# Optimization experiments

Hardware: AMD Instinct MI355X
Metric: run time of the kernel (lower is better)

The kernel has to match this reference:

```python
import jax, jax.numpy as jnp
import numpy as np

IN_CH = 128
OUT_CH = 1
N_NODES = 20000
N_EDGES = 640000
EPS = 1e-5


def setup_inputs() -> dict:
    key = jax.random.key(0)
    ks = jax.random.split(key, 8)
    x = jax.random.normal(ks[0], (N_NODES, IN_CH), dtype=jnp.float32)
    edge_index = jax.random.randint(ks[1], (2, N_EDGES), 0, N_NODES, dtype=jnp.int64)
    s1 = 1.0 / np.sqrt(2 * IN_CH)
    s2 = 1.0 / np.sqrt(IN_CH)
    return {
        "x": x,
        "edge_index": edge_index,
        "W1": jax.random.normal(ks[2], (2 * IN_CH, IN_CH), dtype=jnp.float32) * s1,
        "b1": jnp.zeros((IN_CH,), dtype=jnp.float32),
        "bn_g": jnp.ones((IN_CH,), dtype=jnp.float32),
        "bn_b": jnp.zeros((IN_CH,), dtype=jnp.float32),
        "W2": jax.random.normal(ks[3], (IN_CH, IN_CH), dtype=jnp.float32) * s2,
        "b2": jnp.zeros((IN_CH,), dtype=jnp.float32),
        "ln_g": jnp.ones((IN_CH,), dtype=jnp.float32),
        "ln_b": jnp.zeros((IN_CH,), dtype=jnp.float32),
        "W3": jax.random.normal(ks[4], (IN_CH, OUT_CH), dtype=jnp.float32) * s2,
        "b3": jnp.zeros((OUT_CH,), dtype=jnp.float32),
    }


def gcn_conv(h, src, dst, num_nodes, bias):
    # h: [num_nodes, F] already linearly transformed. GCN norm with self loops:
    # deg[i] = 1 + in-degree(i); norm_e = deg[src]^-1/2 * deg[dst]^-1/2
    deg = jnp.zeros((num_nodes,), h.dtype).at[dst].add(1.0) + 1.0
    dinv = deg ** -0.5
    norm = dinv[src] * dinv[dst]                      # [E]
    agg = jnp.zeros_like(h).at[dst].add(h[src] * norm[:, None])
    agg = agg + h * (dinv * dinv)[:, None]            # self-loop contribution
    return agg + bias


def reference(x, edge_index, W1, b1, bn_g, bn_b, W2, b2, ln_g, ln_b, W3, b3):
    src, dst = edge_index[0], edge_index[1]
    E = src.shape[0]
    # edge features: [E, 2*IN_CH]
    ef = jnp.concatenate([x[src], x[dst]], axis=1)
    # GCNConv 1 over E "nodes" (edge-feature rows)
    h = gcn_conv(ef @ W1, src, dst, E, b1)
    # BatchNorm1d (training-mode batch stats, biased variance)
    mean = h.mean(axis=0)
    var = h.var(axis=0)
    h = (h - mean) * jax.lax.rsqrt(var + EPS) * bn_g + bn_b
    h = jax.nn.relu(h)
    # GCNConv 2
    h = gcn_conv(h @ W2, src, dst, E, b2)
    # LayerNorm over feature dim
    mu = h.mean(axis=-1, keepdims=True)
    v = h.var(axis=-1, keepdims=True)
    h = (h - mu) * jax.lax.rsqrt(v + EPS) * ln_g + ln_b
    h = jax.nn.relu(h)
    out = h @ W3 + b3                                  # [E, 1]
    return out.squeeze()
```

## Files before the change

### kernel.cpp

```cpp
#include <hip/hip_runtime.h>
#include <hip/hip_bf16.h>

#define NN 20000
#define NE 640000
#define TAILN (NE - NN)
#define F  128
#define EPSN 1e-5f

typedef __bf16 bf16;
typedef bf16  bf16x8 __attribute__((ext_vector_type(8)));
typedef bf16  bf16x4 __attribute__((ext_vector_type(4)));
typedef float f32x4  __attribute__((ext_vector_type(4)));
typedef float f32x2  __attribute__((ext_vector_type(2)));
typedef unsigned short u16;

__global__ void k_cvt_idx(const void* __restrict__ ei_raw, int* __restrict__ srcb,
                          int* __restrict__ dstb, int* __restrict__ cnt,
                          int* __restrict__ cst, int* __restrict__ cdt) {
  const int* e32 = (const int*)ei_raw;
  const long long* e64 = (const long long*)ei_raw;
  bool is64 = true;
#pragma unroll
  for (int k = 0; k < 8; ++k) is64 = is64 && (e32[2 * k + 1] == 0);
  int e = blockIdx.x * 256 + threadIdx.x;
  if (e < NE) {
    int s, d;
    if (is64) { s = (int)e64[e]; d = (int)e64[NE + e]; }
    else      { s = e32[e];      d = e32[NE + e]; }
    srcb[e] = s; dstb[e] = d;
    atomicAdd(&cnt[d], 1);
    if (e >= NN) { atomicAdd(&cst[s], 1); atomicAdd(&cdt[d], 1); }
  }
}

__global__ __launch_bounds__(256) void k1_gemm1(const float* __restrict__ x,
        const float* __restrict__ W1, bf16* __restrict__ xa, bf16* __restrict__ xb) {
  __shared__ float XT[64][129];
  int row0 = blockIdx.x * 64;
  int half = blockIdx.y >> 1;
  int cb   = (blockIdx.y & 1) * 64;
  const float* W = W1 + (size_t)half * F * F;
  bf16* out = half ? xb : xa;
  int t = threadIdx.x;
#pragma unroll
  for (int i = 0; i < 8; ++i) {
    int flat = i * 1024 + t * 4;
    int r = flat >> 7, c = flat & 127;
    int gr = row0 + r;
    f32x4 v = {0.f, 0.f, 0.f, 0.f};
    if (gr < NN) v = *(const f32x4*)(x + (size_t)gr * F + c);
    XT[r][c] = v[0]; XT[r][c + 1] = v[1]; XT[r][c + 2] = v[2]; XT[r][c + 3] = v[3];
  }
  __syncthreads();
  int tc = t & 15, tr = t >> 4;
  float acc[4][4] = {};
  for (int k = 0; k < F; ++k) {
    f32x4 wv = *(const f32x4*)(W + (size_t)k * F + cb + tc * 4);
    float x0 = XT[tr * 4 + 0][k], x1 = XT[tr * 4 + 1][k];
    float x2 = XT[tr * 4 + 2][k], x3 = XT[tr * 4 + 3][k];
#pragma unroll
    for (int j = 0; j < 4; ++j) {
      acc[0][j] += x0 * wv[j]; acc[1][j] += x1 * wv[j];
      acc[2][j] += x2 * wv[j]; acc[3][j] += x3 * wv[j];
    }
  }
#pragma unroll
  for (int i = 0; i < 4; ++i) {
    int gr = row0 + tr * 4 + i;
    if (gr < NN) {
      bf16x4 o;
#pragma unroll
      for (int j = 0; j < 4; ++j) o[j] = (bf16)acc[i][j];
      *(bf16x4*)(out + (size_t)gr * F + cb + tc * 4) = o;
    }
  }
}

__global__ __launch_bounds__(1024) void k3_scan(const int* __restrict__ cnt,
        int* __restrict__ ptr, int* __restrict__ cursor,
        float* __restrict__ dinv, float* __restrict__ invdeg) {
  __shared__ int wsum[16];
  __shared__ int carry_s;
  int t = threadIdx.x;
  int lane = t & 63, wv = t >> 6;
  if (t == 0) carry_s = 0;
  __syncthreads();
  for (int c0 = 0; c0 < NN; c0 += 1024) {
    int i = c0 + t;
    int v = (i < NN) ? cnt[i] : 0;
    int s = v;
#pragma unroll
    for (int off = 1; off < 64; off <<= 1) {
      int n = __shfl_up(s, off);
      if (lane >= off) s += n;
    }
    if (lane == 63) wsum[wv] = s;
    __syncthreads();
    int carry = carry_s;
    int wbase = 0;
#pragma unroll
    for (int k2 = 0; k2 < 16; ++k2) wbase += (k2 < wv) ? wsum[k2] : 0;
    int incl = s + wbase;
    if (i < NN) {
      int excl = carry + incl - v;
      ptr[i] = excl; cursor[i] = excl;
      float deg = (float)(v + 1);
      dinv[i] = rsqrtf(deg);
      invdeg[i] = 1.0f / deg;
    }
    __syncthreads();
    if (t == 1023) carry_s = carry + incl;
    __syncthreads();
  }
  if (t == 0) ptr[NN] = carry_s;
}

__global__ void k4_hhead(const int* __restrict__ srcb, const int* __restrict__ dstb,
                         const bf16* __restrict__ xa, const bf16* __restrict__ xb,
                         bf16* __restrict__ hh) {
  int flat = blockIdx.x * 256 + threadIdx.x;
  int j = flat >> 4, ch = flat & 15;
  if (j >= NN) return;
  int s = srcb[j], d = dstb[j];
  bf16x8 a = *(const bf16x8*)(xa + (size_t)s * F + ch * 8);
  bf16x8 b = *(const bf16x8*)(xb + (size_t)d * F + ch * 8);
  bf16x8 o;
#pragma unroll
  for (int m = 0; m < 8; ++m) o[m] = (bf16)((float)a[m] + (float)b[m]);
  *(bf16x8*)(hh + (size_t)j * F + ch * 8) = o;
}

__global__ void k5_fill(const int* __restrict__ srcb, const int* __restrict__ dstb,
                        int* __restrict__ cursor, int* __restrict__ csr_s) {
  int e = blockIdx.x * 256 + threadIdx.x;
  if (e < NE) {
    int d = dstb[e];
    int pos = atomicAdd(&cursor[d], 1);
    csr_s[pos] = srcb[e] | ((e >= NN) ? (1 << 16) : 0);
  }
}

__global__ __launch_bounds__(256) void k6_conv1cross(const int* __restrict__ ptr,
        const int* __restrict__ csr_s, const bf16* __restrict__ hh,
        const bf16* __restrict__ xa, const bf16* __restrict__ xb,
        const float* __restrict__ dinv, const float* __restrict__ invdeg,
        const float* __restrict__ b1, float* __restrict__ h1h,
        float* __restrict__ crossrow) {
  int w = threadIdx.x >> 6, lane = threadIdx.x & 63;
  int g = lane >> 4, k = lane & 15;
  int i = blockIdx.x * 4 + w;
  int c0 = k * 8;
  int beg = ptr[i], end = ptr[i + 1];
  float acc[8] = {0,0,0,0,0,0,0,0}, z[8] = {0,0,0,0,0,0,0,0};
  int q = beg + g;
  for (; q + 4 < end; q += 8) {
    int v0 = csr_s[q], v1 = csr_s[q + 4];
    int s0 = v0 & 0xFFFF, s1 = v1 & 0xFFFF;
    float f0 = (v0 >> 16) ? 1.f : 0.f, f1 = (v1 >> 16) ? 1.f : 0.f;
    float d0 = dinv[s0], d1 = dinv[s1];
    bf16x8 h0 = *(const bf16x8*)(hh + (size_t)s0 * F + c0);
    bf16x8 x0 = *(const bf16x8*)(xa + (size_t)s0 * F + c0);
    bf16x8 h1 = *(const bf16x8*)(hh + (size_t)s1 * F + c0);
    bf16x8 x1 = *(const bf16x8*)(xa + (size_t)s1 * F + c0);
#pragma unroll
    for (int j = 0; j < 8; ++j) {
      acc[j] += d0 * (float)h0[j] + d1 * (float)h1[j];
      z[j]   += f0 * (float)x0[j] + f1 * (float)x1[j];
    }
  }
  if (q < end) {
    int v0 = csr_s[q];
    int s0 = v0 & 0xFFFF;
    float f0 = (v0 >> 16) ? 1.f : 0.f;
    float d0 = dinv[s0];
    bf16x8 h0 = *(const bf16x8*)(hh + (size_t)s0 * F + c0);
    bf16x8 x0 = *(const bf16x8*)(xa + (size_t)s0 * F + c0);
#pragma unroll
    for (int j = 0; j < 8; ++j) {
      acc[j] += d0 * (float)h0[j];
      z[j]   += f0 * (float)x0[j];
    }
  }
#pragma unroll
  for (int m = 16; m < 64; m <<= 1) {
#pragma unroll
    for (int j = 0; j < 8; ++j) {
      acc[j] += __shfl_xor(acc[j], m);
      z[j]   += __shfl_xor(z[j], m);
    }
  }
  if (g == 0) {
    float di = dinv[i], iv = invdeg[i];
    bf16x8 self = *(const bf16x8*)(hh + (size_t)i * F + c0);
    f32x4 bA = *(const f32x4*)(b1 + c0), bB = *(const f32x4*)(b1 + c0 + 4);
    f32x4 o0, o1;
#pragma unroll
    for (int j = 0; j < 4; ++j) {
      o0[j] = di * acc[j]     + (float)self[j]     * iv + bA[j];
      o1[j] = di * acc[j + 4] + (float)self[j + 4] * iv + bB[j];
    }
    *(f32x4*)(h1h + (size_t)i * F + c0) = o0;
    *(f32x4*)(h1h + (size_t)i * F + c0 + 4) = o1;
  } else if (g == 1) {
    bf16x8 xbv = *(const bf16x8*)(xb + (size_t)i * F + c0);
    f32x4 o0, o1;
#pragma unroll
    for (int j = 0; j < 4; ++j) {
      o0[j] = (float)xbv[j]     * z[j];
      o1[j] = (float)xbv[j + 4] * z[j + 4];
    }
    *(f32x4*)(crossrow + (size_t)i * F + c0) = o0;
    *(f32x4*)(crossrow + (size_t)i * F + c0 + 4) = o1;
  }
}

__global__ __launch_bounds__(256) void k7sr(const float* __restrict__ h1h,
        const float* __restrict__ crossrow, const bf16* __restrict__ xa,
        const bf16* __restrict__ xb, const int* __restrict__ cst,
        const int* __restrict__ cdt, float* __restrict__ statsB) {
  int t = threadIdx.x;
  int w = t >> 6, lane = t & 63, k = lane & 15;
  int rg = t >> 4;
  int c0 = k * 8;
  int base = blockIdx.x * 200;
  float A1[8] = {0,0,0,0,0,0,0,0}, A2[8] = {0,0,0,0,0,0,0,0};
  float B1[8] = {0,0,0,0,0,0,0,0}, B2[8] = {0,0,0,0,0,0,0,0};
  float Cc[8] = {0,0,0,0,0,0,0,0};
  for (int r = rg; r < 200; r += 16) {
    int n = base + r;
    f32x4 h0 = *(const f32x4*)(h1h + (size_t)n * F + c0);
    f32x4 h1 = *(const f32x4*)(h1h + (size_t)n * F + c0 + 4);
    f32x4 cr0 = *(const f32x4*)(crossrow + (size_t)n * F + c0);
    f32x4 cr1 = *(const f32x4*)(crossrow + (size_t)n * F + c0 + 4);
    bf16x8 av = *(const bf16x8*)(xa + (size_t)n * F + c0);
    bf16x8 bv = *(const bf16x8*)(xb + (size_t)n * F + c0);
    float ca = (float)cst[n], cb = (float)cdt[n];
#pragma unroll
    for (int j = 0; j < 4; ++j) {
      A1[j] += h0[j]; A2[j] += h0[j] * h0[j];
      A1[j + 4] += h1[j]; A2[j + 4] += h1[j] * h1[j];
      Cc[j] += cr0[j]; Cc[j + 4] += cr1[j];
    }
#pragma unroll
    for (int j = 0; j < 8; ++j) {
      float a = (float)av[j], b = (float)bv[j];
      B1[j] += ca * a + cb * b;
      B2[j] += ca * a * a + cb * b * b;
    }
  }
#pragma unroll
  for (int m = 16; m < 64; m <<= 1) {
#pragma unroll
    for (int j = 0; j < 8; ++j) {
      A1[j] += __shfl_xor(A1[j], m); A2[j] += __shfl_xor(A2[j], m);
      B1[j] += __shfl_xor(B1[j], m); B2[j] += __shfl_xor(B2[j], m);
      Cc[j] += __shfl_xor(Cc[j], m);
    }
  }
  __shared__ float L[4][5][128];
  if (lane < 16) {
#pragma unroll
    for (int j = 0; j < 8; ++j) {
      L[w][0][c0 + j] = A1[j]; L[w][1][c0 + j] = A2[j];
      L[w][2][c0 + j] = B1[j]; L[w][3][c0 + j] = B2[j];
      L[w][4][c0 + j] = Cc[j];
    }
  }
  __syncthreads();
  if (t < 128) {
#pragma unroll
    for (int term = 0; term < 5; ++term) {
      float v = L[0][term][t] + L[1][term][t] + L[2][term][t] + L[3][term][t];
      atomicAdd(&statsB[term * 128 + t], v);
    }
  }
}

__global__ __launch_bounds__(256) void k8_final(const float* __restrict__ statsB,
        const float* __restrict__ bn_g, const float* __restrict__ bn_b,
        const float* __restrict__ b1, const float* __restrict__ W2,
        float* __restrict__ P, float* __restrict__ Qh, float* __restrict__ Qt,
        u16* __restrict__ W2t) {
  int t = threadIdx.x;
  if (t < 128) {
    float A1 = statsB[t], A2 = statsB[128 + t], B1v = statsB[256 + t];
    float B2v = statsB[384 + t], Cv = statsB[512 + t];
    float b1c = b1[t];
    float S = A1 + B1v + (float)TAILN * b1c;
    float Q = A2 + B2v + 2.f * Cv + 2.f * b1c * B1v + (float)TAILN * b1c * b1c;
    float mean = S * (1.0f / NE);
    float var = Q * (1.0f / NE) - mean * mean;
    float rs = rsqrtf(var + EPSN);
    float p = bn_g[t] * rs;
    float sh = bn_b[t] - mean * p;
    P[t] = p; Qh[t] = sh; Qt[t] = p * b1c + sh;
  }
  for (int i = 0; i < 64; ++i) {
    int flat = i * 256 + t;
    int k = flat >> 7, c = flat & 127;
    union { bf16 b; u16 u; } cv;
    cv.b = (bf16)W2[(size_t)k * F + c];
    W2t[(size_t)c * F + k] = cv.u;
  }
}

__global__ __launch_bounds__(256) void k9a_headgemm(const float* __restrict__ h1h,
        const float* __restrict__ P, const float* __restrict__ Qh,
        const u16* __restrict__ W2t, bf16* __restrict__ h2ph) {
  __shared__ __align__(16) bf16 A[64 * 128];
  __shared__ __align__(16) bf16 B[128 * 128];
  int t = threadIdx.x;
  int row0 = blockIdx.x * 64;
  const bf16x8* srcB = (const bf16x8*)W2t;
#pragma unroll
  for (int i = 0; i < 8; ++i) {
    int ch = i * 256 + t;
    int r = ch >> 4, cir = ch & 15;
    *(bf16x8*)&B[r * 128 + ((cir ^ (r & 7)) << 3)] = srcB[ch];
  }
  {
    int r = t >> 2, sub = t & 3;
    int gr = row0 + r;
#pragma unroll
    for (int j = 0; j < 4; ++j) {
      int c0 = sub * 32 + j * 8;
      f32x4 v0 = {0.f,0.f,0.f,0.f}, v1 = {0.f,0.f,0.f,0.f};
      if (gr < NN) {
        v0 = *(const f32x4*)(h1h + (size_t)gr * F + c0);
        v1 = *(const f32x4*)(h1h + (size_t)gr * F + c0 + 4);
      }
      f32x4 p0 = *(const f32x4*)(P + c0), p1 = *(const f32x4*)(P + c0 + 4);
      f32x4 q0 = *(const f32x4*)(Qh + c0), q1 = *(const f32x4*)(Qh + c0 + 4);
      bf16x8 o;
#pragma unroll
      for (int m = 0; m < 4; ++m) {
        o[m]     = (bf16)fmaxf(v0[m] * p0[m] + q0[m], 0.f);
        o[m + 4] = (bf16)fmaxf(v1[m] * p1[m] + q1[m], 0.f);
      }
      int ch = c0 >> 3;
      *(bf16x8*)&A[r * 128 + ((ch ^ (r & 7)) << 3)] = o;
    }
  }
  __syncthreads();
  int lane = t & 63, w = t >> 6;
  int lr = lane & 15, g = lane >> 4;
  int arow = w * 16 + lr;
  bf16x8 af[4];
#pragma unroll
  for (int kk = 0; kk < 4; ++kk)
    af[kk] = *(const bf16x8*)&A[arow * 128 + (((kk * 4 + g) ^ (arow & 7)) << 3)];
  f32x4 acc[8];
#pragma unroll
  for (int n = 0; n < 8; ++n) {
    f32x4 a = {0.f,0.f,0.f,0.f};
    int col = n * 16 + lr;
#pragma unroll
    for (int kk = 0; kk < 4; ++kk) {
      bf16x8 bfr = *(const bf16x8*)&B[col * 128 + (((kk * 4 + g) ^ (col & 7)) << 3)];
      a = __builtin_amdgcn_mfma_f32_16x16x32_bf16(af[kk], bfr, a, 0, 0, 0);
    }
    acc[n] = a;
  }
#pragma unroll
  for (int n = 0; n < 8; ++n) {
#pragma unroll
    for (int r4 = 0; r4 < 4; ++r4) {
      int gr = row0 + w * 16 + g * 4 + r4;
      if (gr < NN) h2ph[(size_t)gr * F + n * 16 + lr] = (bf16)acc[n][r4];
    }
  }
}

__global__ __launch_bounds__(256) void k9b_head(const int* __restrict__ ptr,
        const int* __restrict__ csr_s, const bf16* __restrict__ h2ph,
        const float* __restrict__ dinv, const float* __restrict__ invdeg,
        const float* __restrict__ b2, const float* __restrict__ lng,
        const float* __restrict__ lnb, const float* __restrict__ W3,
        const float* __restrict__ b3, float* __restrict__ out) {
  int w = threadIdx.x >> 6, lane = threadIdx.x & 63;
  int g = lane >> 4, k = lane & 15;
  int i = blockIdx.x * 4 + w;
  int c0 = k * 8;
  int beg = ptr[i], end = ptr[i + 1];
  float acc[8] = {0,0,0,0,0,0,0,0};
  int q = beg + g;
  for (; q + 4 < end; q += 8) {
    int s0 = csr_s[q] & 0xFFFF, s1 = csr_s[q + 4] & 0xFFFF;
    float d0 = dinv[s0], d1 = dinv[s1];
    bf16x8 h0 = *(const bf16x8*)(h2ph + (size_t)s0 * F + c0);
    bf16x8 h1 = *(const bf16x8*)(h2ph + (size_t)s1 * F + c0);
#pragma unroll
    for (int j = 0; j < 8; ++j)
      acc[j] += d0 * (float)h0[j] + d1 * (float)h1[j];
  }
  if (q < end) {
    int s0 = csr_s[q] & 0xFFFF;
    float d0 = dinv[s0];
    bf16x8 h0 = *(const bf16x8*)(h2ph + (size_t)s0 * F + c0);
#pragma unroll
    for (int j = 0; j < 8; ++j) acc[j] += d0 * (float)h0[j];
  }
#pragma unroll
  for (int m = 16; m < 64; m <<= 1) {
#pragma unroll
    for (int j = 0; j < 8; ++j) acc[j] += __shfl_xor(acc[j], m);
  }
  float di = dinv[i], iv = invdeg[i];
  bf16x8 self = *(const bf16x8*)(h2ph + (size_t)i * F + c0);
  f32x4 b2A = *(const f32x4*)(b2 + c0), b2B = *(const f32x4*)(b2 + c0 + 4);
  float h2[8];
#pragma unroll
  for (int j = 0; j < 4; ++j) {
    h2[j]     = di * acc[j]     + (float)self[j]     * iv + b2A[j];
    h2[j + 4] = di * acc[j + 4] + (float)self[j + 4] * iv + b2B[j];
  }
  float s1v = 0.f, s2v = 0.f;
#pragma unroll
  for (int j = 0; j < 8; ++j) { s1v += h2[j]; s2v += h2[j] * h2[j]; }
#pragma unroll
  for (int m = 1; m < 16; m <<= 1) { s1v += __shfl_xor(s1v, m); s2v += __shfl_xor(s2v, m); }
  float mean = s1v * (1.0f / F);
  float var = s2v * (1.0f / F) - mean * mean;
  float rs = rsqrtf(var + EPSN);
  f32x4 lgA = *(const f32x4*)(lng + c0), lgB = *(const f32x4*)(lng + c0 + 4);
  f32x4 lbA = *(const f32x4*)(lnb + c0), lbB = *(const f32x4*)(lnb + c0 + 4);
  f32x4 w3A = *(const f32x4*)(W3 + c0),  w3B = *(const f32x4*)(W3 + c0 + 4);
  float y = 0.f;
#pragma unroll
  for (int j = 0; j < 4; ++j) {
    y += fmaxf((h2[j]     - mean) * rs * lgA[j] + lbA[j], 0.f) * w3A[j];
    y += fmaxf((h2[j + 4] - mean) * rs * lgB[j] + lbB[j], 0.f) * w3B[j];
  }
#pragma unroll
  for (int m = 1; m < 16; m <<= 1) y += __shfl_xor(y, m);
  if (lane == 0) out[i] = y + b3[0];
}

__global__ __launch_bounds__(256) void k9c_tail(const int* __restrict__ srcb,
        const int* __restrict__ dstb, const bf16* __restrict__ xa,
        const bf16* __restrict__ xb, const float* __restrict__ P,
        const float* __restrict__ Qt, const u16* __restrict__ W2t,
        const float* __restrict__ b2, const float* __restrict__ lng,
        const float* __restrict__ lnb, const float* __restrict__ W3,
        const float* __restrict__ b3, float* __restrict__ out) {
  __shared__ __align__(16) bf16 B[128 * 128];
  int t = threadIdx.x;
  const bf16x8* srcB = (const bf16x8*)W2t;
#pragma unroll
  for (int i = 0; i < 8; ++i) {
    int ch = i * 256 + t;
    int r = ch >> 4, cir = ch & 15;
    *(bf16x8*)&B[r * 128 + ((cir ^ (r & 7)) << 3)] = srcB[ch];
  }
  __syncthreads();
  int lane = t & 63, w = t >> 6;
  int lr = lane & 15, g = lane >> 4;
  int ebase = NN + blockIdx.x * 256 + w * 64;
  float b2v[8], lgv[8], lbv[8], w3v[8];
#pragma unroll
  for (int n = 0; n < 8; ++n) {
    int cc = n * 16 + lr;
    b2v[n] = b2[cc]; lgv[n] = lng[cc]; lbv[n] = lnb[cc]; w3v[n] = W3[cc];
  }
  float b3v = b3[0];
  for (int rc = 0; rc < 4; ++rc) {
    int e = ebase + rc * 16 + lr;
    bool ok = (e < NE);
    int se = 0, de = 0;
    if (ok) { se = srcb[e]; de = dstb[e]; }
    bf16x8 af[4];
#pragma unroll
    for (int kk = 0; kk < 4; ++kk) {
      int c0 = kk * 32 + g * 8;
      bf16x8 o;
      if (ok) {
        bf16x8 av = *(const bf16x8*)(xa + (size_t)se * F + c0);
        bf16x8 bv = *(const bf16x8*)(xb + (size_t)de * F + c0);
        f32x4 p0 = *(const f32x4*)(P + c0), p1 = *(const f32x4*)(P + c0 + 4);
        f32x4 q0 = *(const f32x4*)(Qt + c0), q1 = *(const f32x4*)(Qt + c0 + 4);
#pragma unroll
        for (int m = 0; m < 4; ++m) {
          o[m]     = (bf16)fmaxf(((float)av[m] + (float)bv[m]) * p0[m] + q0[m], 0.f);
          o[m + 4] = (bf16)fmaxf(((float)av[m + 4] + (float)bv[m + 4]) * p1[m] + q1[m], 0.f);
        }
      } else {
#pragma unroll
        for (int m = 0; m < 8; ++m) o[m] = (bf16)0.f;
      }
      af[kk] = o;
    }
    f32x4 acc[8];
#pragma unroll
    for (int n = 0; n < 8; ++n) {
      f32x4 a = {0.f,0.f,0.f,0.f};
      int col = n * 16 + lr;
#pragma unroll
      for (int kk = 0; kk < 4; ++kk) {
        bf16x8 bfr = *(const bf16x8*)&B[col * 128 + (((kk * 4 + g) ^ (col & 7)) << 3)];
        a = __builtin_amdgcn_mfma_f32_16x16x32_bf16(af[kk], bfr, a, 0, 0, 0);
      }
      acc[n] = a;
    }
#pragma unroll
    for (int r4 = 0; r4 < 4; ++r4) {
      float vv[8];
      float s = 0.f, q = 0.f;
#pragma unroll
      for (int n = 0; n < 8; ++n) {
        float v = acc[n][r4] + b2v[n];
        vv[n] = v; s += v; q += v * v;
      }
#pragma unroll
      for (int m = 1; m < 16; m <<= 1) { s += __shfl_xor(s, m); q += __shfl_xor(q, m); }
      float mean = s * (1.0f / F);
      float var = q * (1.0f / F) - mean * mean;
      float rs = rsqrtf(var + EPSN);
      float o = 0.f;
#pragma unroll
      for (int n = 0; n < 8; ++n)
        o += fmaxf((vv[n] - mean) * rs * lgv[n] + lbv[n], 0.f) * w3v[n];
#pragma unroll
      for (int m = 1; m < 16; m <<= 1) o += __shfl_xor(o, m);
      int eo = ebase + rc * 16 + g * 4 + r4;
      if (lr == 0 && eo < NE) out[eo] = o + b3v;
    }
  }
}

extern "C" void kernel_launch(void* const* d_in, const int* in_sizes, int n_in,
                              void* d_out, int out_size, void* d_ws, size_t ws_size,
                              hipStream_t stream) {
  const float* x   = (const float*)d_in[0];
  const void*  ei  = d_in[1];
  const float* W1  = (const float*)d_in[2];
  const float* b1  = (const float*)d_in[3];
  const float* bng = (const float*)d_in[4];
  const float* bnb = (const float*)d_in[5];
  const float* W2  = (const float*)d_in[6];
  const float* b2  = (const float*)d_in[7];
  const float* lng = (const float*)d_in[8];
  const float* lnb = (const float*)d_in[9];
  const float* W3  = (const float*)d_in[10];
  const float* b3  = (const float*)d_in[11];
  float* out = (float*)d_out;

  char* ws = (char*)d_ws;
  size_t off = 0;
  auto alloc = [&](size_t bytes) -> char* {
    off = (off + 511) & ~(size_t)511;
    char* p = ws + off;
    off += bytes;
    return p;
  };
  const size_t NFh = (size_t)NN * F * 2;
  bf16*  xa     = (bf16*)alloc(NFh);
  bf16*  xb     = (bf16*)alloc(NFh);
  bf16*  hh     = (bf16*)alloc(NFh);
  float* h1h    = (float*)alloc((size_t)NN * F * 4);
  float* crossr = (float*)alloc((size_t)NN * F * 4);
  int*   srcb   = (int*)alloc((size_t)NE * 4);
  int*   dstb   = (int*)alloc((size_t)NE * 4);
  int*   csr_s  = (int*)alloc((size_t)NE * 4);
  int*   cnt    = (int*)alloc((size_t)NN * 4);
  int*   cst    = (int*)alloc((size_t)NN * 4);
  int*   cdt    = (int*)alloc((size_t)NN * 4);
  int*   ptrb   = (int*)alloc((size_t)(NN + 1) * 4);
  int*   cursor = (int*)alloc((size_t)NN * 4);
  float* dinv   = (float*)alloc((size_t)NN * 4);
  float* invdeg = (float*)alloc((size_t)NN * 4);
  float* statsB = (float*)alloc(5 * 128 * 4);
  float* Pp     = (float*)alloc(128 * 4);
  float* Qh     = (float*)alloc(128 * 4);
  float* Qt     = (float*)alloc(128 * 4);
  u16*   W2t    = (u16*)alloc((size_t)F * F * 2);
  bf16*  h2ph   = hh;

  hipMemsetAsync(cnt, 0, (size_t)NN * 4, stream);
  hipMemsetAsync(cst, 0, (size_t)NN * 4, stream);
  hipMemsetAsync(cdt, 0, (size_t)NN * 4, stream);
  hipMemsetAsync(statsB, 0, 5 * 128 * 4, stream);

  k_cvt_idx<<<2500, 256, 0, stream>>>(ei, srcb, dstb, cnt, cst, cdt);
  k1_gemm1<<<dim3(313, 4), 256, 0, stream>>>(x, W1, xa, xb);
  k3_scan<<<1, 1024, 0, stream>>>(cnt, ptrb, cursor, dinv, invdeg);
  k4_hhead<<<1250, 256, 0, stream>>>(srcb, dstb, xa, xb, hh);
  k5_fill<<<2500, 256, 0, stream>>>(srcb, dstb, cursor, csr_s);
  k6_conv1cross<<<5000, 256, 0, stream>>>(ptrb, csr_s, hh, xa, xb, dinv, invdeg, b1,
                                          h1h, crossr);
  k7sr<<<100, 256, 0, stream>>>(h1h, crossr, xa, xb, cst, cdt, statsB);
  k8_final<<<1, 256, 0, stream>>>(statsB, bng, bnb, b1, W2, Pp, Qh, Qt, W2t);
  k9a_headgemm<<<313, 256, 0, stream>>>(h1h, Pp, Qh, W2t, h2ph);
  k9b_head<<<5000, 256, 0, stream>>>(ptrb, csr_s, h2ph, dinv, invdeg, b2, lng, lnb,
                                     W3, b3, out);
  k9c_tail<<<2422, 256, 0, stream>>>(srcb, dstb, xa, xb, Pp, Qt, W2t, b2, lng, lnb,
                                     W3, b3, out);
}
```

Before: 464.7 us.

## Sort tail edges by destination to improve gather locality in tail kernel

Adds a second counting-sort pass that groups tail edges (e >= NN) by destination node, storing packed src|dst and the original edge id. The tail GEMM kernel then processes edges in destination order, so xb row gathers are reused from cache, and it scatters each output back through the stored edge id. It also packs the b2/ln_g/ln_b/W3 parameters into float4s, which are reloaded inside the loop instead of held in registers. The costs are extra atomics and writes in the fill kernel, a scattered output write, and a longer scan.

New measurement: 591.7 us. 1.27x slower.

```diff
diff --git a/kernel.cpp b/kernel.cpp
--- a/kernel.cpp
+++ b/kernel.cpp
@@ -77,39 +77,46 @@
 }
 
 __global__ __launch_bounds__(1024) void k3_scan(const int* __restrict__ cnt,
-        int* __restrict__ ptr, int* __restrict__ cursor,
-        float* __restrict__ dinv, float* __restrict__ invdeg) {
-  __shared__ int wsum[16];
-  __shared__ int carry_s;
+        const int* __restrict__ cdt, int* __restrict__ ptr, int* __restrict__ cursor,
+        float* __restrict__ dinv, float* __restrict__ invdeg,
+        int* __restrict__ tcursor) {
+  __shared__ int wsum[16], wsum2[16];
+  __shared__ int carry_s, carry2_s;
   int t = threadIdx.x;
   int lane = t & 63, wv = t >> 6;
-  if (t == 0) carry_s = 0;
+  if (t == 0) { carry_s = 0; carry2_s = 0; }
   __syncthreads();
   for (int c0 = 0; c0 < NN; c0 += 1024) {
     int i = c0 + t;
-    int v = (i < NN) ? cnt[i] : 0;
-    int s = v;
+    int v  = (i < NN) ? cnt[i] : 0;
+    int vt = (i < NN) ? cdt[i] : 0;
+    int s = v, st = vt;
 #pragma unroll
     for (int off = 1; off < 64; off <<= 1) {
-      int n = __shfl_up(s, off);
-      if (lane >= off) s += n;
-    }
-    if (lane == 63) wsum[wv] = s;
+      int n1 = __shfl_up(s, off);
+      int n2 = __shfl_up(st, off);
+      if (lane >= off) { s += n1; st += n2; }
+    }
+    if (lane == 63) { wsum[wv] = s; wsum2[wv] = st; }
     __syncthreads();
-    int carry = carry_s;
-    int wbase = 0;
-#pragma unroll
-    for (int k2 = 0; k2 < 16; ++k2) wbase += (k2 < wv) ? wsum[k2] : 0;
-    int incl = s + wbase;
+    int carry = carry_s, carry2 = carry2_s;
+    int wbase = 0, wbase2 = 0;
+#pragma unroll
+    for (int k2 = 0; k2 < 16; ++k2) {
+      wbase  += (k2 < wv) ? wsum[k2]  : 0;
+      wbase2 += (k2 < wv) ? wsum2[k2] : 0;
+    }
+    int incl = s + wbase, incl2 = st + wbase2;
     if (i < NN) {
       int excl = carry + incl - v;
       ptr[i] = excl; cursor[i] = excl;
+      tcursor[i] = carry2 + incl2 - vt;
       float deg = (float)(v + 1);
       dinv[i] = rsqrtf(deg);
       invdeg[i] = 1.0f / deg;
     }
     __syncthreads();
-    if (t == 1023) carry_s = carry + incl;
+    if (t == 1023) { carry_s = carry + incl; carry2_s = carry2 + incl2; }
     __syncthreads();
   }
   if (t == 0) ptr[NN] = carry_s;
@@ -131,12 +138,19 @@
 }
 
 __global__ void k5_fill(const int* __restrict__ srcb, const int* __restrict__ dstb,
-                        int* __restrict__ cursor, int* __restrict__ csr_s) {
+                        int* __restrict__ cursor, int* __restrict__ tcursor,
+                        int* __restrict__ csr_s, int* __restrict__ csr_td,
+                        int* __restrict__ csr_te) {
   int e = blockIdx.x * 256 + threadIdx.x;
   if (e < NE) {
-    int d = dstb[e];
+    int s = srcb[e], d = dstb[e];
     int pos = atomicAdd(&cursor[d], 1);
-    csr_s[pos] = srcb[e] | ((e >= NN) ? (1 << 16) : 0);
+    csr_s[pos] = s | ((e >= NN) ? (1 << 16) : 0);
+    if (e >= NN) {
+      int p2 = atomicAdd(&tcursor[d], 1);
+      csr_td[p2] = s | (d << 16);
+      csr_te[p2] = e;
+    }
   }
 }
 
@@ -279,8 +293,10 @@
 __global__ __launch_bounds__(256) void k8_final(const float* __restrict__ statsB,
         const float* __restrict__ bn_g, const float* __restrict__ bn_b,
         const float* __restrict__ b1, const float* __restrict__ W2,
+        const float* __restrict__ b2, const float* __restrict__ lng,
+        const float* __restrict__ lnb, const float* __restrict__ W3,
         float* __restrict__ P, float* __restrict__ Qh, float* __restrict__ Qt,
-        u16* __restrict__ W2t) {
+        u16* __restrict__ W2t, f32x4* __restrict__ params4) {
   int t = threadIdx.x;
   if (t < 128) {
     float A1 = statsB[t], A2 = statsB[128 + t], B1v = statsB[256 + t];
@@ -294,6 +310,8 @@
     float p = bn_g[t] * rs;
     float sh = bn_b[t] - mean * p;
     P[t] = p; Qh[t] = sh; Qt[t] = p * b1c + sh;
+    f32x4 pr = {b2[t], lng[t], lnb[t], W3[t]};
+    params4[t] = pr;
   }
   for (int i = 0; i < 64; ++i) {
     int flat = i * 256 + t;
@@ -436,13 +454,12 @@
   if (lane == 0) out[i] = y + b3[0];
 }
 
-__global__ __launch_bounds__(256) void k9c_tail(const int* __restrict__ srcb,
-        const int* __restrict__ dstb, const bf16* __restrict__ xa,
+__global__ __launch_bounds__(256) void k9c_tail(const int* __restrict__ csr_td,
+        const int* __restrict__ csr_te, const bf16* __restrict__ xa,
         const bf16* __restrict__ xb, const float* __restrict__ P,
         const float* __restrict__ Qt, const u16* __restrict__ W2t,
-        const float* __restrict__ b2, const float* __restrict__ lng,
-        const float* __restrict__ lnb, const float* __restrict__ W3,
-        const float* __restrict__ b3, float* __restrict__ out) {
+        const f32x4* __restrict__ params4, const float* __restrict__ b3,
+        float* __restrict__ out) {
   __shared__ __align__(16) bf16 B[128 * 128];
   int t = threadIdx.x;
   const bf16x8* srcB = (const bf16x8*)W2t;
@@ -455,37 +472,29 @@
   __syncthreads();
   int lane = t & 63, w = t >> 6;
   int lr = lane & 15, g = lane >> 4;
-  int ebase = NN + blockIdx.x * 256 + w * 64;
-  float b2v[8], lgv[8], lbv[8], w3v[8];
-#pragma unroll
-  for (int n = 0; n < 8; ++n) {
-    int cc = n * 16 + lr;
-    b2v[n] = b2[cc]; lgv[n] = lng[cc]; lbv[n] = lnb[cc]; w3v[n] = W3[cc];
+  int pbase = blockIdx.x * 256 + w * 64;
+  int pk[4];
+#pragma unroll
+  for (int rc = 0; rc < 4; ++rc) {
+    int p = pbase + rc * 16 + lr;
+    pk[rc] = (p < TAILN) ? csr_td[p] : 0;
   }
   float b3v = b3[0];
   for (int rc = 0; rc < 4; ++rc) {
-    int e = ebase + rc * 16 + lr;
-    bool ok = (e < NE);
-    int se = 0, de = 0;
-    if (ok) { se = srcb[e]; de = dstb[e]; }
+    int se = pk[rc] & 0xFFFF, de = ((unsigned)pk[rc]) >> 16;
     bf16x8 af[4];
 #pragma unroll
     for (int kk = 0; kk < 4; ++kk) {
       int c0 = kk * 32 + g * 8;
+      bf16x8 av = *(const bf16x8*)(xa + (size_t)se * F + c0);
+      bf16x8 bv = *(const bf16x8*)(xb + (size_t)de * F + c0);
+      f32x4 p0 = *(const f32x4*)(P + c0), p1 = *(const f32x4*)(P + c0 + 4);
+      f32x4 q0 = *(const f32x4*)(Qt + c0), q1 = *(const f32x4*)(Qt + c0 + 4);
       bf16x8 o;
-      if (ok) {
-        bf16x8 av = *(const bf16x8*)(xa + (size_t)se * F + c0);
-        bf16x8 bv = *(const bf16x8*)(xb + (size_t)de * F + c0);
-        f32x4 p0 = *(const f32x4*)(P + c0), p1 = *(const f32x4*)(P + c0 + 4);
-        f32x4 q0 = *(const f32x4*)(Qt + c0), q1 = *(const f32x4*)(Qt + c0 + 4);
-#pragma unroll
-        for (int m = 0; m < 4; ++m) {
-          o[m]     = (bf16)fmaxf(((float)av[m] + (float)bv[m]) * p0[m] + q0[m], 0.f);
-          o[m + 4] = (bf16)fmaxf(((float)av[m + 4] + (float)bv[m + 4]) * p1[m] + q1[m], 0.f);
-        }
-      } else {
-#pragma unroll
-        for (int m = 0; m < 8; ++m) o[m] = (bf16)0.f;
+#pragma unroll
+      for (int m = 0; m < 4; ++m) {
+        o[m]     = (bf16)fmaxf(((float)av[m] + (float)bv[m]) * p0[m] + q0[m], 0.f);
+        o[m + 4] = (bf16)fmaxf(((float)av[m + 4] + (float)bv[m + 4]) * p1[m] + q1[m], 0.f);
       }
       af[kk] = o;
     }
@@ -507,7 +516,8 @@
       float s = 0.f, q = 0.f;
 #pragma unroll
       for (int n = 0; n < 8; ++n) {
-        float v = acc[n][r4] + b2v[n];
+        f32x4 pr = params4[n * 16 + lr];
+        float v = acc[n][r4] + pr[0];
         vv[n] = v; s += v; q += v * v;
       }
 #pragma unroll
@@ -517,12 +527,14 @@
       float rs = rsqrtf(var + EPSN);
       float o = 0.f;
 #pragma unroll
-      for (int n = 0; n < 8; ++n)
-        o += fmaxf((vv[n] - mean) * rs * lgv[n] + lbv[n], 0.f) * w3v[n];
+      for (int n = 0; n < 8; ++n) {
+        f32x4 pr = params4[n * 16 + lr];
+        o += fmaxf((vv[n] - mean) * rs * pr[1] + pr[2], 0.f) * pr[3];
+      }
 #pragma unroll
       for (int m = 1; m < 16; m <<= 1) o += __shfl_xor(o, m);
-      int eo = ebase + rc * 16 + g * 4 + r4;
-      if (lr == 0 && eo < NE) out[eo] = o + b3v;
+      int po = pbase + rc * 16 + g * 4 + r4;
+      if (lr == 0 && po < TAILN) out[csr_te[po]] = o + b3v;
     }
   }
 }
@@ -561,11 +573,14 @@
   int*   srcb   = (int*)alloc((size_t)NE * 4);
   int*   dstb   = (int*)alloc((size_t)NE * 4);
   int*   csr_s  = (int*)alloc((size_t)NE * 4);
+  int*   csr_td = (int*)alloc((size_t)TAILN * 4);
+  int*   csr_te = (int*)alloc((size_t)TAILN * 4);
   int*   cnt    = (int*)alloc((size_t)NN * 4);
   int*   cst    = (int*)alloc((size_t)NN * 4);
   int*   cdt    = (int*)alloc((size_t)NN * 4);
   int*   ptrb   = (int*)alloc((size_t)(NN + 1) * 4);
   int*   cursor = (int*)alloc((size_t)NN * 4);
+  int*   tcursor= (int*)alloc((size_t)NN * 4);
   float* dinv   = (float*)alloc((size_t)NN * 4);
   float* invdeg = (float*)alloc((size_t)NN * 4);
   float* statsB = (float*)alloc(5 * 128 * 4);
@@ -573,6 +588,7 @@
   float* Qh     = (float*)alloc(128 * 4);
   float* Qt     = (float*)alloc(128 * 4);
   u16*   W2t    = (u16*)alloc((size_t)F * F * 2);
+  f32x4* params4= (f32x4*)alloc(128 * 16);
   bf16*  h2ph   = hh;
 
   hipMemsetAsync(cnt, 0, (size_t)NN * 4, stream);
@@ -582,16 +598,17 @@
 
   k_cvt_idx<<<2500, 256, 0, stream>>>(ei, srcb, dstb, cnt, cst, cdt);
   k1_gemm1<<<dim3(313, 4), 256, 0, stream>>>(x, W1, xa, xb);
-  k3_scan<<<1, 1024, 0, stream>>>(cnt, ptrb, cursor, dinv, invdeg);
+  k3_scan<<<1, 1024, 0, stream>>>(cnt, cdt, ptrb, cursor, dinv, invdeg, tcursor);
   k4_hhead<<<1250, 256, 0, stream>>>(srcb, dstb, xa, xb, hh);
-  k5_fill<<<2500, 256, 0, stream>>>(srcb, dstb, cursor, csr_s);
+  k5_fill<<<2500, 256, 0, stream>>>(srcb, dstb, cursor, tcursor, csr_s, csr_td, csr_te);
   k6_conv1cross<<<5000, 256, 0, stream>>>(ptrb, csr_s, hh, xa, xb, dinv, invdeg, b1,
                                           h1h, crossr);
   k7sr<<<100, 256, 0, stream>>>(h1h, crossr, xa, xb, cst, cdt, statsB);
-  k8_final<<<1, 256, 0, stream>>>(statsB, bng, bnb, b1, W2, Pp, Qh, Qt, W2t);
+  k8_final<<<1, 256, 0, stream>>>(statsB, bng, bnb, b1, W2, b2, lng, lnb, W3,
+                                  Pp, Qh, Qt, W2t, params4);
   k9a_headgemm<<<313, 256, 0, stream>>>(h1h, Pp, Qh, W2t, h2ph);
   k9b_head<<<5000, 256, 0, stream>>>(ptrb, csr_s, h2ph, dinv, invdeg, b2, lng, lnb,
                                      W3, b3, out);
-  k9c_tail<<<2422, 256, 0, stream>>>(srcb, dstb, xa, xb, Pp, Qt, W2t, b2, lng, lnb,
-                                     W3, b3, out);
-}
+  k9c_tail<<<2423, 256, 0, stream>>>(csr_td, csr_te, xa, xb, Pp, Qt, W2t, params4,
+                                     b3, out);
+}
```
